# Performance work log

Measured on AMD Instinct MI355X. Metric: run time of the kernel, lower is better.

The kernel has to match this reference:

```python
import jax, jax.numpy as jnp
import numpy as np

B, M, N = 32, 512, 512
XD = YD = 512   # x_size, y_size
S = 512         # shared_size
H = 512         # hidden_size
MAXD = 11       # max relative distance


def _lin(k, i, o):
    lim = float(np.sqrt(6.0 / (i + o)))  # xavier_uniform, gain=1
    return jax.random.uniform(k, (i, o), jnp.float32, -lim, lim)


def setup_inputs() -> dict:
    key = jax.random.key(0)
    ks = jax.random.split(key, 16)
    inp = {
        'prem': jax.random.normal(ks[0], (B, M, YD), jnp.float32),
        'hypo': jax.random.normal(ks[1], (B, N, XD), jnp.float32),
        'prem_mask': jnp.ones((B, M), dtype=bool),
        'hypo_mask': jnp.ones((B, N), dtype=bool),
        # projections
        'Wpx': _lin(ks[2], XD, S), 'bpx': jnp.zeros((S,), jnp.float32),
        'Wpy': _lin(ks[3], YD, S), 'bpy': jnp.zeros((S,), jnp.float32),
        # relative-distance bias embedding (2*max_dist+1, squeezed to scalar)
        'dist_embed': jax.random.normal(ks[4], (2 * MAXD + 1,), jnp.float32),
        # self-attention DeepDot MLP: S -> H -> H
        'Ws1': _lin(ks[5], S, H), 'bs1': jnp.zeros((H,), jnp.float32),
        'Ws2': _lin(ks[6], H, H), 'bs2': jnp.zeros((H,), jnp.float32),
        # cross-attention DeepDot MLP: 2S -> H -> H
        'Wa1': _lin(ks[7], 2 * S, H), 'ba1': jnp.zeros((H,), jnp.float32),
        'Wa2': _lin(ks[8], H, H), 'ba2': jnp.zeros((H,), jnp.float32),
        # compare layer: 4S -> H -> H
        'Wc1': _lin(ks[9], 4 * S, H), 'bc1': jnp.zeros((H,), jnp.float32),
        'Wc2': _lin(ks[10], H, H), 'bc2': jnp.zeros((H,), jnp.float32),
        # aggregate layer: 2H -> H -> H
        'Wg1': _lin(ks[11], 2 * H, H), 'bg1': jnp.zeros((H,), jnp.float32),
        'Wg2': _lin(ks[12], H, H), 'bg2': jnp.zeros((H,), jnp.float32),
    }
    return inp


def _mlp2(x, W1, b1, W2, b2):
    # Linear -> ReLU -> Linear -> ReLU (dropout=0.0)
    h = jax.nn.relu(x @ W1 + b1)
    return jax.nn.relu(h @ W2 + b2)


def _rel_bias(size, dist_embed):
    v = jnp.arange(size)
    d = jnp.clip(v[None, :] - v[:, None], -MAXD, MAXD) + MAXD  # [size,size]
    return dist_embed[d]


def _masked_softmax(t, mask):
    # mask True = valid; broadcast over query dim
    return jax.nn.softmax(jnp.where(mask, t, -jnp.inf), axis=-1)


def reference(prem, hypo, prem_mask, hypo_mask,
              Wpx, bpx, Wpy, bpy, dist_embed,
              Ws1, bs1, Ws2, bs2,
              Wa1, ba1, Wa2, ba2,
              Wc1, bc1, Wc2, bc2,
              Wg1, bg1, Wg2, bg2):
    hypo_p = hypo @ Wpx + bpx   # [B,N,S]
    prem_p = prem @ Wpy + bpy   # [B,M,S]

    # self attention (DeepDot: shared MLP on q and k, then qk^T)
    fp = _mlp2(prem_p, Ws1, bs1, Ws2, bs2)
    fh = _mlp2(hypo_p, Ws1, bs1, Ws2, bs2)
    p_scores = jnp.einsum('bmh,bnh->bmn', fp, fp) + _rel_bias(prem_p.shape[1], dist_embed)[None]
    h_scores = jnp.einsum('bmh,bnh->bmn', fh, fh) + _rel_bias(hypo_p.shape[1], dist_embed)[None]

    p_att = _masked_softmax(p_scores, prem_mask[:, None, :])
    h_att = _masked_softmax(h_scores, hypo_mask[:, None, :])
    prem_ctx = jnp.einsum('bmn,bnd->bmd', p_att, prem_p)
    hypo_ctx = jnp.einsum('bmn,bnd->bmd', h_att, hypo_p)

    prem2 = jnp.concatenate([prem_p, prem_ctx], axis=-1)  # [B,M,2S]
    hypo2 = jnp.concatenate([hypo_p, hypo_ctx], axis=-1)  # [B,N,2S]

    # cross attention
    gp = _mlp2(prem2, Wa1, ba1, Wa2, ba2)
    gh = _mlp2(hypo2, Wa1, ba1, Wa2, ba2)
    sim = jnp.einsum('bmh,bnh->bmn', gp, gh)  # [B,M,N]
    p2h = _masked_softmax(sim, hypo_mask[:, None, :])
    h2p = _masked_softmax(jnp.swapaxes(sim, 1, 2), prem_mask[:, None, :])
    attended_hypo = jnp.einsum('bmn,bnd->bmd', p2h, hypo2)  # [B,M,2S]
    attended_prem = jnp.einsum('bnm,bmd->bnd', h2p, prem2)  # [B,N,2S]

    prem_cmp = _mlp2(jnp.concatenate([prem2, attended_hypo], -1), Wc1, bc1, Wc2, bc2)
    hypo_cmp = _mlp2(jnp.concatenate([hypo2, attended_prem], -1), Wc1, bc1, Wc2, bc2)

    prem_cmp = (prem_cmp * prem_mask[..., None].astype(prem_cmp.dtype)).sum(axis=1)  # [B,H]
    hypo_cmp = (hypo_cmp * hypo_mask[..., None].astype(hypo_cmp.dtype)).sum(axis=1)  # [B,H]

    return _mlp2(jnp.concatenate([prem_cmp, hypo_cmp], -1), Wg1, bg1, Wg2, bg2)
```

## Files before the change

kernel.cpp:

```cpp
#include <hip/hip_runtime.h>
#include <hip/hip_bf16.h>


typedef __bf16 bf16x8 __attribute__((ext_vector_type(8)));
typedef float floatx16 __attribute__((ext_vector_type(16)));
typedef float floatx4 __attribute__((ext_vector_type(4)));

__device__ __forceinline__ unsigned short f32_to_bf16(float f) {
    unsigned int u = __float_as_uint(f);
    unsigned int r = (u + 0x7FFFu + ((u >> 16) & 1u)) >> 16;
    return (unsigned short)r;
}
__device__ __forceinline__ float bf16_to_f32(unsigned short h) {
    return __uint_as_float(((unsigned int)h) << 16);
}

__device__ __forceinline__ void gload16(const void* g, void* l) {
    __builtin_amdgcn_global_load_lds(
        (const __attribute__((address_space(1))) unsigned int*)g,
        (__attribute__((address_space(3))) unsigned int*)l, 16, 0, 0);
}

#define FENCE_BAR() do { asm volatile("" ::: "memory"); \
    __builtin_amdgcn_s_barrier(); \
    asm volatile("" ::: "memory"); } while (0)

struct TW {
    const float* src[8];
    unsigned short* dst[8];
    int K[8];
};
__global__ __launch_bounds__(256) void transpose_all_kernel(TW tw) {
    const int z = blockIdx.z;
    const int K = tw.K[z];
    const int k0 = blockIdx.y * 32;
    if (k0 >= K) return;
    const float* W = tw.src[z];
    unsigned short* Wt = tw.dst[z];
    __shared__ unsigned short tile[32][33];
    int n0 = blockIdx.x * 32;
    int tx = threadIdx.x & 31, ty = threadIdx.x >> 5;
    #pragma unroll
    for (int i = 0; i < 4; ++i) {
        int ky = ty + i * 8;
        tile[ky][tx] = f32_to_bf16(W[(long long)(k0 + ky) * 512 + n0 + tx]);
    }
    __syncthreads();
    #pragma unroll
    for (int i = 0; i < 4; ++i) {
        int ny = ty + i * 8;
        Wt[(long long)(n0 + ny) * K + k0 + tx] = tile[tx][ny];
    }
}

template <bool BT, bool AF32>
__global__ __launch_bounds__(256, 4) void gemm_kernel(
    const void* __restrict__ Av, const void* __restrict__ A2v, int lda, long long strideA,
    const unsigned short* __restrict__ Bw, int ldb, long long strideB, int bxor,
    const unsigned short* __restrict__ B2, const float* __restrict__ bias2, int Msplit,
    float* __restrict__ C32, unsigned short* __restrict__ Cb, int ldc, long long strideC,
    const float* __restrict__ bias, int relu, int M, int N, int K,
    float* __restrict__ csum, int swz) {
    constexpr int BBYTES = BT ? 8192 : (32 * 264);
    constexpr int BUF = 8192 + BBYTES;
    __shared__ alignas(16) char smem[2 * BUF];

    const int t = threadIdx.x;
    const int lane = t & 63;
    const int wave = t >> 6;
    const int wm = (wave >> 1) * 64;
    const int wn = (wave & 1) * 64;
    const int ln = lane & 31;
    const int h = lane >> 5;

    int bx = blockIdx.x, by = blockIdx.y, bz = blockIdx.z;
    if (swz == 1) {
        int Nt = gridDim.x, Mt = gridDim.y;
        int L = by * Nt + bx;
        int x = L & 7, s = L >> 3;
        by = x * (Mt >> 3) + s / Nt;
        bx = s % Nt;
    } else if (swz == 2) {
        int Nt = gridDim.x, Mt = gridDim.y;
        int L = (bz * Mt + by) * Nt + bx;
        int x = L & 7, s = L >> 3;
        int mg = x * ((Mt * (int)gridDim.z) >> 3) + s / Nt;
        bx = s % Nt;
        by = mg % Mt;
        bz = mg / Mt;
    }
    const int m0 = by * 128;
    const int n0 = bx * 128;
    const int bzB = (bz + bxor) & ((int)gridDim.z - 1);

    const unsigned short* B = Bw;
    const float* biasp = bias;
    long long mA = m0;
    if (Msplit && m0 >= Msplit) {
        if (B2) B = B2;
        if (bias2) biasp = bias2;
        if (A2v) { Av = A2v; mA = m0 - Msplit; }
    }

    const float* aptrF = nullptr;
    const unsigned short* aptrH = nullptr;
    if constexpr (AF32)
        aptrF = (const float*)Av + (long long)bz * strideA +
                (mA + (t >> 1)) * (long long)lda + (t & 1) * 16;
    else
        aptrH = (const unsigned short*)Av + (long long)bz * strideA +
                (mA + (t >> 1)) * (long long)lda + (t & 1) * 16;
    const unsigned short* bptr;
    if (BT)
        bptr = B + (long long)bzB * strideB +
               (long long)(n0 + (t >> 1)) * ldb + (t & 1) * 16;
    else
        bptr = B + (long long)bzB * strideB +
               (long long)(t >> 4) * ldb + n0 + (t & 15) * 8;
    const long long bstep = BT ? 8 : 16 * (long long)ldb;

    const int aoff = ((t & 1) * 256 + (t >> 1)) * 16;
    const int boff = BT ? (8192 + ((t & 1) * 256 + (t >> 1)) * 16)
                        : (8192 + (t >> 4) * 264 + (t & 15) * 16);
    const int boff2 = BT ? 2048 : 16 * 264;

    floatx16 acc[2][2];
    #pragma unroll
    for (int im = 0; im < 2; ++im)
        #pragma unroll
        for (int in = 0; in < 2; ++in)
            acc[im][in] = (floatx16)(0.f);

    uint4 va0, va1, vb0, vb1;
    float4 fa0, fa1, fa2, fa3;

    auto loadA = [&]() {
        if constexpr (AF32) {
            fa0 = *(const float4*)(aptrF);
            fa1 = *(const float4*)(aptrF + 4);
            fa2 = *(const float4*)(aptrF + 8);
            fa3 = *(const float4*)(aptrF + 12);
            aptrF += 32;
        } else {
            va0 = *(const uint4*)(aptrH);
            va1 = *(const uint4*)(aptrH + 8);
            aptrH += 32;
        }
    };
    auto loadB = [&]() {
        vb0 = *(const uint4*)(bptr);
        vb1 = *(const uint4*)(bptr + bstep);
        bptr += BT ? 32 : 32 * (long long)ldb;
    };
    auto commit = [&](char* buf) {
        if constexpr (AF32) {
            union { uint4 q; unsigned short u[8]; } c0, c1;
            c0.u[0] = f32_to_bf16(fa0.x); c0.u[1] = f32_to_bf16(fa0.y);
            c0.u[2] = f32_to_bf16(fa0.z); c0.u[3] = f32_to_bf16(fa0.w);
            c0.u[4] = f32_to_bf16(fa1.x); c0.u[5] = f32_to_bf16(fa1.y);
            c0.u[6] = f32_to_bf16(fa1.z); c0.u[7] = f32_to_bf16(fa1.w);
            c1.u[0] = f32_to_bf16(fa2.x); c1.u[1] = f32_to_bf16(fa2.y);
            c1.u[2] = f32_to_bf16(fa2.z); c1.u[3] = f32_to_bf16(fa2.w);
            c1.u[4] = f32_to_bf16(fa3.x); c1.u[5] = f32_to_bf16(fa3.y);
            c1.u[6] = f32_to_bf16(fa3.z); c1.u[7] = f32_to_bf16(fa3.w);
            *(uint4*)(buf + aoff) = c0.q;
            *(uint4*)(buf + aoff + 2048) = c1.q;
        } else {
            *(uint4*)(buf + aoff) = va0;
            *(uint4*)(buf + aoff + 2048) = va1;
        }
        *(uint4*)(buf + boff) = vb0;
        *(uint4*)(buf + boff + boff2) = vb1;
    };

    loadA(); loadB();
    commit(smem);
    loadA(); loadB();
    __syncthreads();

    int p = 0;
    for (int k0 = 0; k0 < K; k0 += 32) {
        const char* base = smem + p * BUF;
        #pragma unroll
        for (int s = 0; s < 2; ++s) {
            bf16x8 a[2], b[2];
            #pragma unroll
            for (int im = 0; im < 2; ++im)
                a[im] = *(const bf16x8*)(base + ((s * 2 + h) * 128 + wm + im * 32 + ln) * 16);
            if (BT) {
                #pragma unroll
                for (int in = 0; in < 2; ++in)
                    b[in] = *(const bf16x8*)(base + 8192 +
                                             ((s * 2 + h) * 128 + wn + in * 32 + ln) * 16);
            } else {
                #pragma unroll
                for (int in = 0; in < 2; ++in) {
                    union { bf16x8 v; unsigned short u[8]; } u;
                    #pragma unroll
                    for (int j = 0; j < 8; ++j)
                        u.u[j] = *(const unsigned short*)(base + 8192 +
                                 (s * 16 + h * 8 + j) * 264 + (wn + in * 32 + ln) * 2);
                    b[in] = u.v;
                }
            }
            #pragma unroll
            for (int im = 0; im < 2; ++im)
                #pragma unroll
                for (int in = 0; in < 2; ++in)
                    acc[im][in] = __builtin_amdgcn_mfma_f32_32x32x16_bf16(
                        a[im], b[in], acc[im][in], 0, 0, 0);
        }

        if (k0 + 32 < K) {
            commit(smem + (p ^ 1) * BUF);
            if (k0 + 64 < K) { loadA(); loadB(); }
            __syncthreads();
            p ^= 1;
        }
    }

    if (csum) {
        const int bidx = m0 >> 9;
        const long long cbase = (long long)(bidx & 31) * 1024 + (bidx >> 5) * 512;
        #pragma unroll
        for (int in = 0; in < 2; ++in) {
            int n = n0 + wn + in * 32 + ln;
            float bn = biasp ? biasp[n] : 0.f;
            float s = 0.f;
            #pragma unroll
            for (int im = 0; im < 2; ++im)
                #pragma unroll
                for (int r = 0; r < 16; ++r) {
                    float v = acc[im][in][r] + bn;
                    if (relu) v = fmaxf(v, 0.f);
                    s += v;
                }
            s += __shfl_xor(s, 32);
            if (lane < 32) atomicAdd(&csum[cbase + n], s);
        }
        return;
    }

    float* C32b = C32 ? C32 + (long long)bz * strideC : nullptr;
    unsigned short* Cbb = Cb ? Cb + (long long)bz * strideC : nullptr;
    #pragma unroll
    for (int im = 0; im < 2; ++im) {
        #pragma unroll
        for (int in = 0; in < 2; ++in) {
            int n = n0 + wn + in * 32 + ln;
            float bn = biasp ? biasp[n] : 0.f;
            #pragma unroll
            for (int r = 0; r < 16; ++r) {
                int m = m0 + wm + im * 32 + (r & 3) + 8 * (r >> 2) + 4 * h;
                float v = acc[im][in][r] + bn;
                if (relu) v = fmaxf(v, 0.f);
                long long off = (long long)m * ldc + n;
                if (C32b) C32b[off] = v;
                if (Cbb) Cbb[off] = f32_to_bf16(v);
            }
        }
    }
}

__global__ __launch_bounds__(512, 2) void gemm256_kernel(
    const unsigned short* __restrict__ Aw, int lda, long long strideA,
    const unsigned short* __restrict__ Bw, int ldb, long long strideB, int bxor,
    float* __restrict__ C32, unsigned short* __restrict__ Cb, int ldc, long long strideC,
    const float* __restrict__ bias, int relu, int K) {
    extern __shared__ __align__(16) char smem[];

    const int tid = threadIdx.x;
    const int lane = tid & 63;
    const int wave = tid >> 6;
    const int wr = wave >> 2;
    const int wc = wave & 3;

    int bx = blockIdx.x, by = blockIdx.y, bz = blockIdx.z;
    {
        const int gx = gridDim.x, gy = gridDim.y;
        const int nwg = gx * gy * (int)gridDim.z;
        if ((nwg & 7) == 0) {
            int L = (bz * gy + by) * gx + bx;
            int flat = (L & 7) * (nwg >> 3) + (L >> 3);
            bx = flat % gx;
            int R = flat / gx;
            by = R % gy;
            bz = R / gy;
        }
    }
    const int m0 = by * 256;
    const int n0 = bx * 256;
    const int bzB = (bz + bxor) & ((int)gridDim.z - 1);

    const int rowT = tid >> 3;
    const int chS = (tid & 7) ^ (rowT & 7);
    const long long ldaB = (long long)lda * 2;
    const long long ldbB = (long long)ldb * 2;
    const char* aG = (const char*)Aw +
        ((long long)bz * strideA + (long long)(m0 + rowT) * lda) * 2 + chS * 16;
    const char* bG = (const char*)Bw +
        ((long long)bzB * strideB + (long long)(n0 + rowT) * ldb) * 2 + chS * 16;
    const int dOff = tid * 16;

    auto stA = [&](int tt, int h) {
        const char* g = aG + (long long)(h * 128) * ldaB + (long long)tt * 128;
        char* l = smem + (tt & 1) * 65536 + h * 16384 + dOff;
        gload16(g, l);
        gload16(g + 64 * ldaB, l + 8192);
    };
    auto stB = [&](int tt, int h) {
        const char* g = bG + (long long)(h * 128) * ldbB + (long long)tt * 128;
        char* l = smem + (tt & 1) * 65536 + 32768 + h * 16384 + dOff;
        gload16(g, l);
        gload16(g + 64 * ldbB, l + 8192);
    };

    const int l15 = lane & 15;
    const int lk = lane >> 4;
    const int swzb = (lane & 7) << 4;
    const int c0 = (lk * 16) ^ swzb;
    const int c1 = (64 + lk * 16) ^ swzb;
    const int arow = (wr * 128 + l15) * 128;
    const int brow = 32768 + (wc * 64 + l15) * 128;

    floatx4 acc[8][4];
    #pragma unroll
    for (int mf = 0; mf < 8; ++mf)
        #pragma unroll
        for (int nf = 0; nf < 4; ++nf)
            acc[mf][nf] = (floatx4)(0.f);

    const int NT = K >> 6;

    stA(0, 0); stA(0, 1); stB(0, 0); stB(0, 1);
    if (NT > 1) {
        stB(1, 0); stB(1, 1);
        asm volatile("s_waitcnt vmcnt(4)" ::: "memory");
    } else {
        asm volatile("s_waitcnt vmcnt(0)" ::: "memory");
    }
    FENCE_BAR();

    bf16x8 a[4][2], b[4][2];
    for (int t = 0; t < NT; ++t) {
        const char* buf = smem + (t & 1) * 65536;
        const char* aB = buf + arow;
        const char* bB = buf + brow;

        #pragma unroll
        for (int mf = 0; mf < 4; ++mf) {
            a[mf][0] = *(const bf16x8*)(aB + mf * 2048 + c0);
            a[mf][1] = *(const bf16x8*)(aB + mf * 2048 + c1);
        }
        #pragma unroll
        for (int nf = 0; nf < 2; ++nf) {
            b[nf][0] = *(const bf16x8*)(bB + nf * 2048 + c0);
            b[nf][1] = *(const bf16x8*)(bB + nf * 2048 + c1);
        }
        if (t + 1 < NT) stA(t + 1, 0);
        FENCE_BAR();
        __builtin_amdgcn_s_setprio(1);
        #pragma unroll
        for (int mf = 0; mf < 4; ++mf)
            #pragma unroll
            for (int nf = 0; nf < 2; ++nf) {
                acc[mf][nf] = __builtin_amdgcn_mfma_f32_16x16x32_bf16(
                    a[mf][0], b[nf][0], acc[mf][nf], 0, 0, 0);
                acc[mf][nf] = __builtin_amdgcn_mfma_f32_16x16x32_bf16(
                    a[mf][1], b[nf][1], acc[mf][nf], 0, 0, 0);
            }
        __builtin_amdgcn_s_setprio(0);
        FENCE_BAR();

        #pragma unroll
        for (int nf = 2; nf < 4; ++nf) {
            b[nf][0] = *(const bf16x8*)(bB + nf * 2048 + c0);
            b[nf][1] = *(const bf16x8*)(bB + nf * 2048 + c1);
        }
        if (t + 1 < NT) stA(t + 1, 1);
        FENCE_BAR();
        __builtin_amdgcn_s_setprio(1);
        #pragma unroll
        for (int mf = 0; mf < 4; ++mf)
            #pragma unroll
            for (int nf = 2; nf < 4; ++nf) {
                acc[mf][nf] = __builtin_amdgcn_mfma_f32_16x16x32_bf16(
                    a[mf][0], b[nf][0], acc[mf][nf], 0, 0, 0);
                acc[mf][nf] = __builtin_amdgcn_mfma_f32_16x16x32_bf16(
                    a[mf][1], b[nf][1], acc[mf][nf], 0, 0, 0);
            }
        __builtin_amdgcn_s_setprio(0);
        FENCE_BAR();

        #pragma unroll
        for (int mf = 0; mf < 4; ++mf) {
            a[mf][0] = *(const bf16x8*)(aB + (4 + mf) * 2048 + c0);
            a[mf][1] = *(const bf16x8*)(aB + (4 + mf) * 2048 + c1);
        }
        if (t + 2 < NT) stB(t + 2, 0);
        FENCE_BAR();
        __builtin_amdgcn_s_setprio(1);
        #pragma unroll
        for (int mf = 0; mf < 4; ++mf)
            #pragma unroll
            for (int nf = 2; nf < 4; ++nf) {
                acc[4 + mf][nf] = __builtin_amdgcn_mfma_f32_16x16x32_bf16(
                    a[mf][0], b[nf][0], acc[4 + mf][nf], 0, 0, 0);
                acc[4 + mf][nf] = __builtin_amdgcn_mfma_f32_16x16x32_bf16(
                    a[mf][1], b[nf][1], acc[4 + mf][nf], 0, 0, 0);
            }
        __builtin_amdgcn_s_setprio(0);
        FENCE_BAR();

        if (t + 2 < NT) {
            stB(t + 2, 1);
            asm volatile("s_waitcnt vmcnt(4)" ::: "memory");
        } else {
            asm volatile("s_waitcnt vmcnt(0)" ::: "memory");
        }
        FENCE_BAR();
        __builtin_amdgcn_s_setprio(1);
        #pragma unroll
        for (int mf = 0; mf < 4; ++mf)
            #pragma unroll
            for (int nf = 0; nf < 2; ++nf) {
                acc[4 + mf][nf] = __builtin_amdgcn_mfma_f32_16x16x32_bf16(
                    a[mf][0], b[nf][0], acc[4 + mf][nf], 0, 0, 0);
                acc[4 + mf][nf] = __builtin_amdgcn_mfma_f32_16x16x32_bf16(
                    a[mf][1], b[nf][1], acc[4 + mf][nf], 0, 0, 0);
            }
        __builtin_amdgcn_s_setprio(0);
        FENCE_BAR();
    }

    const int rg = (lane >> 4) * 4;
    float* C32b = C32 ? C32 + (long long)bz * strideC : nullptr;
    unsigned short* Cbb = Cb ? Cb + (long long)bz * strideC : nullptr;
    #pragma unroll
    for (int nf = 0; nf < 4; ++nf) {
        const int n = n0 + wc * 64 + nf * 16 + l15;
        const float bn = bias ? bias[n] : 0.f;
        #pragma unroll
        for (int mf = 0; mf < 8; ++mf) {
            #pragma unroll
            for (int r = 0; r < 4; ++r) {
                int m = m0 + wr * 128 + mf * 16 + rg + r;
                float v = acc[mf][nf][r] + bn;
                if (relu) v = fmaxf(v, 0.f);
                long long off = (long long)m * ldc + n;
                if (C32b) C32b[off] = v;
                if (Cbb) Cbb[off] = f32_to_bf16(v);
            }
        }
    }
}

__global__ __launch_bounds__(256, 2) void attn_kernel(
    const unsigned short* __restrict__ F,
    int bxor,
    unsigned short* __restrict__ att,
    const float* __restrict__ de, int rel) {
    constexpr int BUF = 36864;
    __shared__ alignas(16) char smem[2 * BUF];
    __shared__ alignas(16) float red[2][64][4];
    __shared__ float deL[23];

    const int t = threadIdx.x;
    const int lane = t & 63;
    const int wave = t >> 6;
    const int ln = lane & 31;
    const int h = lane >> 5;

    const int orig = blockIdx.y * (int)gridDim.x + blockIdx.x;
    const int xcd = orig & 7;
    const int s8 = orig >> 3;
    const int by = s8 & 7;
    const int bz = xcd + ((s8 >> 3) << 3);
    const int m0 = by * 64;
    const int bzB = (bz + bxor) & 63;

    if (t < 23) deL[t] = de[t];

    const unsigned short* aptr = F + (long long)bz * (512 * 512) +
                                 (m0 + (t >> 2)) * 512 + (t & 3) * 8;
    const unsigned short* bptr = F + (long long)bzB * (512 * 512) +
                                 (t >> 1) * 512 + (t & 1) * 16;
    const int aoff = ((t & 3) * 64 + (t >> 2)) * 16;
    const int c2 = (t & 1) * 2;
    const int brow = (t >> 1) * 16;

    floatx16 acc[2][4];
    #pragma unroll
    for (int mf = 0; mf < 2; ++mf)
        #pragma unroll
        for (int nf = 0; nf < 4; ++nf)
            acc[mf][nf] = (floatx16)(0.f);

    uint4 qa, q0a, q0b, q1a, q1b, q2a, q2b, q3a, q3b;
    auto load = [&]() {
        qa  = *(const uint4*)(aptr);
        q0a = *(const uint4*)(bptr);
        q0b = *(const uint4*)(bptr + 8);
        q1a = *(const uint4*)(bptr + 65536);
        q1b = *(const uint4*)(bptr + 65536 + 8);
        q2a = *(const uint4*)(bptr + 131072);
        q2b = *(const uint4*)(bptr + 131072 + 8);
        q3a = *(const uint4*)(bptr + 196608);
        q3b = *(const uint4*)(bptr + 196608 + 8);
        aptr += 32; bptr += 32;
    };
    auto commit = [&](char* buf) {
        *(uint4*)(buf + aoff) = qa;
        char* bb = buf + 4096;
        *(uint4*)(bb + (c2 + 0) * 8192 + brow) = q0a;
        *(uint4*)(bb + (c2 + 1) * 8192 + brow) = q0b;
        *(uint4*)(bb + (c2 + 0) * 8192 + brow + 128 * 16) = q1a;
        *(uint4*)(bb + (c2 + 1) * 8192 + brow + 128 * 16) = q1b;
        *(uint4*)(bb + (c2 + 0) * 8192 + brow + 256 * 16) = q2a;
        *(uint4*)(bb + (c2 + 1) * 8192 + brow + 256 * 16) = q2b;
        *(uint4*)(bb + (c2 + 0) * 8192 + brow + 384 * 16) = q3a;
        *(uint4*)(bb + (c2 + 1) * 8192 + brow + 384 * 16) = q3b;
    };

    load(); commit(smem); load();
    __syncthreads();

    int p = 0;
    for (int k0 = 0; k0 < 512; k0 += 32) {
        const char* buf = smem + p * BUF;
        #pragma unroll
        for (int s = 0; s < 2; ++s) {
            bf16x8 a[2], b[4];
            #pragma unroll
            for (int mf = 0; mf < 2; ++mf)
                a[mf] = *(const bf16x8*)(buf + ((s * 2 + h) * 64 + mf * 32 + ln) * 16);
            #pragma unroll
            for (int nf = 0; nf < 4; ++nf)
                b[nf] = *(const bf16x8*)(buf + 4096 + (s * 2 + h) * 8192 +
                                         (wave * 128 + nf * 32 + ln) * 16);
            #pragma unroll
            for (int mf = 0; mf < 2; ++mf)
                #pragma unroll
                for (int nf = 0; nf < 4; ++nf)
                    acc[mf][nf] = __builtin_amdgcn_mfma_f32_32x32x16_bf16(
                        a[mf], b[nf], acc[mf][nf], 0, 0, 0);
        }
        if (k0 + 32 < 512) {
            commit(smem + (p ^ 1) * BUF);
            if (k0 + 64 < 512) load();
            __syncthreads();
            p ^= 1;
        }
    }

    if (rel) {
        #pragma unroll
        for (int mf = 0; mf < 2; ++mf)
            #pragma unroll
            for (int nf = 0; nf < 4; ++nf)
                #pragma unroll
                for (int r = 0; r < 16; ++r) {
                    int row = m0 + mf * 32 + (r & 3) + 8 * (r >> 2) + 4 * h;
                    int col = wave * 128 + nf * 32 + ln;
                    int d = min(11, max(-11, col - row));
                    acc[mf][nf][r] += deL[d + 11];
                }
    }

    #pragma unroll
    for (int mf = 0; mf < 2; ++mf)
        #pragma unroll
        for (int r = 0; r < 16; ++r) {
            float mx = fmaxf(fmaxf(acc[mf][0][r], acc[mf][1][r]),
                             fmaxf(acc[mf][2][r], acc[mf][3][r]));
            #pragma unroll
            for (int o = 16; o > 0; o >>= 1) mx = fmaxf(mx, __shfl_xor(mx, o));
            if (ln == 0)
                red[0][mf * 32 + (r & 3) + 8 * (r >> 2) + 4 * h][wave] = mx;
        }
    __syncthreads();

    #pragma unroll
    for (int mf = 0; mf < 2; ++mf)
        #pragma unroll
        for (int r = 0; r < 16; ++r) {
            const int rl = mf * 32 + (r & 3) + 8 * (r >> 2) + 4 * h;
            float4 q = *(const float4*)red[0][rl];
            float mx = fmaxf(fmaxf(q.x, q.y), fmaxf(q.z, q.w));
            float s = 0.f;
            #pragma unroll
            for (int nf = 0; nf < 4; ++nf) {
                acc[mf][nf][r] = __expf(acc[mf][nf][r] - mx);
                s += acc[mf][nf][r];
            }
            #pragma unroll
            for (int o = 16; o > 0; o >>= 1) s += __shfl_xor(s, o);
            if (ln == 0) red[1][rl][wave] = s;
        }
    __syncthreads();

    unsigned short* ab = att + ((long long)bz * 512 + m0) * 1024;
    #pragma unroll
    for (int mf = 0; mf < 2; ++mf)
        #pragma unroll
        for (int r = 0; r < 16; ++r) {
            const int rl = mf * 32 + (r & 3) + 8 * (r >> 2) + 4 * h;
            float4 q = *(const float4*)red[1][rl];
            float inv = 1.f / (q.x + q.y + q.z + q.w);
            #pragma unroll
            for (int nf = 0; nf < 4; ++nf) {
                int col = wave * 128 + nf * 32 + ln;
                ab[(long long)rl * 1024 + col] = f32_to_bf16(acc[mf][nf][r] * inv);
            }
        }
}

__global__ __launch_bounds__(512) void mlp_agg_kernel(const float* __restrict__ X,
                                                      const float* __restrict__ W,
                                                      const float* __restrict__ bias,
                                                      float* __restrict__ out,
                                                      int K, int N, int relu) {
    const int b = blockIdx.y;
    const int nl = threadIdx.x & 63;
    const int n = blockIdx.x * 64 + nl;
    const int ks = threadIdx.x >> 6;
    const int kchunk = K >> 3;
    const float* Xb = X + (long long)b * K;
    const int k0 = ks * kchunk;
    float s = 0.f;
    #pragma unroll 8
    for (int k = k0; k < k0 + kchunk; ++k)
        s += Xb[k] * W[(long long)k * N + n];
    __shared__ float red[8][64];
    red[ks][nl] = s;
    __syncthreads();
    if (threadIdx.x < 64) {
        float t = 0.f;
        #pragma unroll
        for (int i = 0; i < 8; ++i) t += red[i][threadIdx.x];
        t += bias[n];
        if (relu) t = fmaxf(t, 0.f);
        out[(long long)b * N + n] = t;
    }
}

static void gemm(hipStream_t st, bool bt, bool af32,
                 const void* A, const void* A2, int lda, long long sA,
                 const void* B, int ldb, long long sB, int bxor,
                 const void* B2, const float* bias2, int Msplit,
                 float* C32, void* Cb, int ldc, long long sC,
                 const float* bias, int relu, int M, int N, int K, int batch,
                 float* csum = nullptr) {
    dim3 g(N / 128, M / 128, batch), blk(256);
    int swz = 0;
    if (batch == 1 && (M / 128) % 8 == 0) swz = 1;
    else if (batch > 1 && ((M / 128) * batch) % 8 == 0) swz = 2;
    if (bt) {
        if (af32)
            gemm_kernel<true, true><<<g, blk, 0, st>>>(
                A, A2, lda, sA, (const unsigned short*)B, ldb, sB, bxor,
                (const unsigned short*)B2, bias2, Msplit,
                C32, (unsigned short*)Cb, ldc, sC, bias, relu, M, N, K, csum, swz);
        else
            gemm_kernel<true, false><<<g, blk, 0, st>>>(
                A, A2, lda, sA, (const unsigned short*)B, ldb, sB, bxor,
                (const unsigned short*)B2, bias2, Msplit,
                C32, (unsigned short*)Cb, ldc, sC, bias, relu, M, N, K, csum, swz);
    } else {
        gemm_kernel<false, false><<<g, blk, 0, st>>>(
            A, A2, lda, sA, (const unsigned short*)B, ldb, sB, bxor,
            (const unsigned short*)B2, bias2, Msplit,
            C32, (unsigned short*)Cb, ldc, sC, bias, relu, M, N, K, csum, swz);
    }
}

static void gemm256(hipStream_t st,
                    const void* A, int lda, long long sA,
                    const void* B, int ldb, long long sB, int bxor,
                    float* C32, void* Cb, int ldc, long long sC,
                    const float* bias, int relu, int M, int N, int K, int batch) {
    static bool inited = false;
    if (!inited) {
        hipFuncSetAttribute(reinterpret_cast<const void*>(gemm256_kernel),
                            hipFuncAttributeMaxDynamicSharedMemorySize, 131072);
        inited = true;
    }
    dim3 g(N / 256, M / 256, batch);
    gemm256_kernel<<<g, 512, 131072, st>>>(
        (const unsigned short*)A, lda, sA,
        (const unsigned short*)B, ldb, sB, bxor,
        C32, (unsigned short*)Cb, ldc, sC, bias, relu, K);
}

extern "C" void kernel_launch(void* const* d_in, const int* in_sizes, int n_in,
                              void* d_out, int out_size, void* d_ws, size_t ws_size,
                              hipStream_t stream) {
    const int B = 32, SEQ = 512;
    const int MT = B * SEQ;
    const int M2 = 2 * MT;

    const float* prem = (const float*)d_in[0];
    const float* hypo = (const float*)d_in[1];
    const float* Wpx = (const float*)d_in[4];  const float* bpx = (const float*)d_in[5];
    const float* Wpy = (const float*)d_in[6];  const float* bpy = (const float*)d_in[7];
    const float* de  = (const float*)d_in[8];
    const float* Ws1 = (const float*)d_in[9];  const float* bs1 = (const float*)d_in[10];
    const float* Ws2 = (const float*)d_in[11]; const float* bs2 = (const float*)d_in[12];
    const float* Wa1 = (const float*)d_in[13]; const float* ba1 = (const float*)d_in[14];
    const float* Wa2 = (const float*)d_in[15]; const float* ba2 = (const float*)d_in[16];
    const float* Wc1 = (const float*)d_in[17]; const float* bc1 = (const float*)d_in[18];
    const float* Wc2 = (const float*)d_in[19]; const float* bc2 = (const float*)d_in[20];
    const float* Wg1 = (const float*)d_in[21]; const float* bg1 = (const float*)d_in[22];
    const float* Wg2 = (const float*)d_in[23]; const float* bg2 = (const float*)d_in[24];

    char* p = (char*)d_ws;
    auto alloc = [&](size_t bytes) { char* r = p; p += (bytes + 255) & ~(size_t)255; return r; };
    unsigned short* prem_bf = (unsigned short*)alloc((size_t)MT * 512 * 2);
    unsigned short* hypo_bf = (unsigned short*)alloc((size_t)MT * 512 * 2);
    unsigned short* premcat = (unsigned short*)alloc((size_t)MT * 2048 * 2);
    unsigned short* hypocat = (unsigned short*)alloc((size_t)MT * 2048 * 2);
    float* scores = (float*)alloc((size_t)64 * SEQ * SEQ * 4);
    unsigned short* h1 = (unsigned short*)scores;
    unsigned short* att = (unsigned short*)scores;
    unsigned short* Wpx_t = (unsigned short*)alloc(512 * 512 * 2);
    unsigned short* Wpy_t = (unsigned short*)alloc(512 * 512 * 2);
    unsigned short* Ws1_t = (unsigned short*)alloc(512 * 512 * 2);
    unsigned short* Ws2_t = (unsigned short*)alloc(512 * 512 * 2);
    unsigned short* Wa1_t = (unsigned short*)alloc(512 * 1024 * 2);
    unsigned short* Wa2_t = (unsigned short*)alloc(512 * 512 * 2);
    unsigned short* Wc1_t = (unsigned short*)alloc(512 * 2048 * 2);
    unsigned short* Wc2_t = (unsigned short*)alloc(512 * 512 * 2);
    float* agg  = (float*)alloc(32 * 1024 * 4);
    float* aggh = (float*)alloc(32 * 512 * 4);
    (void)hypo_bf; (void)hypocat; (void)scores;

    const long long sBM = (long long)SEQ * SEQ;
    const long long sAtt = (long long)SEQ * 1024;
    const long long sCat = (long long)SEQ * 2048;

    {
        TW tw;
        tw.src[0] = Wpy; tw.dst[0] = Wpy_t; tw.K[0] = 512;
        tw.src[1] = Wpx; tw.dst[1] = Wpx_t; tw.K[1] = 512;
        tw.src[2] = Ws1; tw.dst[2] = Ws1_t; tw.K[2] = 512;
        tw.src[3] = Ws2; tw.dst[3] = Ws2_t; tw.K[3] = 512;
        tw.src[4] = Wa1; tw.dst[4] = Wa1_t; tw.K[4] = 1024;
        tw.src[5] = Wa2; tw.dst[5] = Wa2_t; tw.K[5] = 512;
        tw.src[6] = Wc1; tw.dst[6] = Wc1_t; tw.K[6] = 2048;
        tw.src[7] = Wc2; tw.dst[7] = Wc2_t; tw.K[7] = 512;
        transpose_all_kernel<<<dim3(16, 64, 8), 256, 0, stream>>>(tw);
        hipMemsetAsync(agg, 0, 32 * 1024 * sizeof(float), stream);
    }

    gemm(stream, true, true, prem, hypo, 512, 0, Wpy_t, 512, 0, 0,
         Wpx_t, bpx, MT, nullptr, premcat, 2048, 0, bpy, 0, M2, 512, 512, 1);

    gemm256(stream, premcat, 2048, 0, Ws1_t, 512, 0, 0,
            nullptr, h1, 512, 0, bs1, 1, M2, 512, 512, 1);
    gemm256(stream, h1, 512, 0, Ws2_t, 512, 0, 0,
            nullptr, prem_bf, 512, 0, bs2, 1, M2, 512, 512, 1);

    attn_kernel<<<dim3(8, 64), 256, 0, stream>>>(prem_bf, 0, att, de, 1);
    gemm(stream, false, false, att, nullptr, 1024, sAtt, premcat, 2048, sCat, 0,
         nullptr, nullptr, 0, nullptr, premcat + 512, 2048, sCat, nullptr, 0, 512, 512, 512, 64);

    gemm256(stream, premcat, 2048, 0, Wa1_t, 1024, 0, 0,
            nullptr, h1, 512, 0, ba1, 1, M2, 512, 1024, 1);
    gemm256(stream, h1, 512, 0, Wa2_t, 512, 0, 0,
            nullptr, prem_bf, 512, 0, ba2, 1, M2, 512, 512, 1);

    attn_kernel<<<dim3(8, 64), 256, 0, stream>>>(prem_bf, 32, att, de, 0);
    gemm(stream, false, false, att, nullptr, 1024, sAtt, premcat, 2048, sCat, 32,
         nullptr, nullptr, 0, nullptr, premcat + 1024, 2048, sCat, nullptr, 0, 512, 1024, 512, 64);

    gemm256(stream, premcat, 2048, 0, Wc1_t, 2048, 0, 0,
            nullptr, h1, 512, 0, bc1, 1, M2, 512, 2048, 1);
    gemm(stream, true, false, h1, nullptr, 512, 0, Wc2_t, 512, 0, 0,
         nullptr, nullptr, 0, nullptr, nullptr, 512, 0, bc2, 1, M2, 512, 512, 1, agg);

    mlp_agg_kernel<<<dim3(8, 32), 512, 0, stream>>>(agg, Wg1, bg1, aggh, 1024, 512, 1);
    mlp_agg_kernel<<<dim3(8, 32), 512, 0, stream>>>(aggh, Wg2, bg2, (float*)d_out, 512, 512, 1);
}
```

Before: 622.2 us.

## Fuse softmax probabilities with the PV matmul in one attention kernel

Result: slower. 673.9 us (+8.3%).

```diff
diff --git a/kernel.cpp b/kernel.cpp
--- a/kernel.cpp
+++ b/kernel.cpp
@@ -455,14 +455,25 @@
     }
 }
 
-__global__ __launch_bounds__(256, 2) void attn_kernel(
+template <bool CROSS>
+__global__ __launch_bounds__(512, 1) void attnpv_kernel(
     const unsigned short* __restrict__ F,
+    const unsigned short* __restrict__ Vsrc,
     int bxor,
-    unsigned short* __restrict__ att,
+    unsigned short* __restrict__ ctxout,
     const float* __restrict__ de, int rel) {
-    constexpr int BUF = 36864;
-    __shared__ alignas(16) char smem[2 * BUF];
-    __shared__ alignas(16) float red[2][64][4];
+    constexpr int D   = CROSS ? 1024 : 512;
+    constexpr int KS  = CROSS ? 16 : 32;
+    constexpr int NS  = 512 / KS;
+    constexpr int VP  = CROSS ? 2080 : 1056;
+    constexpr int DS  = CROSS ? 4 : 2;
+    constexpr int WD  = CROSS ? 128 : 64;
+    constexpr int PBASE = 66560;
+    constexpr int VBYTES = KS * VP;
+    constexpr int SBUF = 36864;
+
+    extern __shared__ __align__(16) char smem[];
+    __shared__ float red[2][64][8];
     __shared__ float deL[23];
 
     const int t = threadIdx.x;
@@ -483,43 +494,33 @@
 
     const unsigned short* aptr = F + (long long)bz * (512 * 512) +
                                  (m0 + (t >> 2)) * 512 + (t & 3) * 8;
-    const unsigned short* bptr = F + (long long)bzB * (512 * 512) +
-                                 (t >> 1) * 512 + (t & 1) * 16;
+    const unsigned short* bptr = F + (long long)bzB * (512 * 512) + t * 512;
     const int aoff = ((t & 3) * 64 + (t >> 2)) * 16;
-    const int c2 = (t & 1) * 2;
-    const int brow = (t >> 1) * 16;
-
-    floatx16 acc[2][4];
+    const int boffB = t * 16;
+
+    floatx16 acc[2][2];
     #pragma unroll
     for (int mf = 0; mf < 2; ++mf)
         #pragma unroll
-        for (int nf = 0; nf < 4; ++nf)
+        for (int nf = 0; nf < 2; ++nf)
             acc[mf][nf] = (floatx16)(0.f);
 
-    uint4 qa, q0a, q0b, q1a, q1b, q2a, q2b, q3a, q3b;
+    uint4 qa, qb0, qb1, qb2, qb3;
     auto load = [&]() {
-        qa  = *(const uint4*)(aptr);
-        q0a = *(const uint4*)(bptr);
-        q0b = *(const uint4*)(bptr + 8);
-        q1a = *(const uint4*)(bptr + 65536);
-        q1b = *(const uint4*)(bptr + 65536 + 8);
-        q2a = *(const uint4*)(bptr + 131072);
-        q2b = *(const uint4*)(bptr + 131072 + 8);
-        q3a = *(const uint4*)(bptr + 196608);
-        q3b = *(const uint4*)(bptr + 196608 + 8);
+        if (t < 256) qa = *(const uint4*)(aptr);
+        qb0 = *(const uint4*)(bptr);
+        qb1 = *(const uint4*)(bptr + 8);
+        qb2 = *(const uint4*)(bptr + 16);
+        qb3 = *(const uint4*)(bptr + 24);
         aptr += 32; bptr += 32;
     };
     auto commit = [&](char* buf) {
-        *(uint4*)(buf + aoff) = qa;
+        if (t < 256) *(uint4*)(buf + aoff) = qa;
         char* bb = buf + 4096;
-        *(uint4*)(bb + (c2 + 0) * 8192 + brow) = q0a;
-        *(uint4*)(bb + (c2 + 1) * 8192 + brow) = q0b;
-        *(uint4*)(bb + (c2 + 0) * 8192 + brow + 128 * 16) = q1a;
-        *(uint4*)(bb + (c2 + 1) * 8192 + brow + 128 * 16) = q1b;
-        *(uint4*)(bb + (c2 + 0) * 8192 + brow + 256 * 16) = q2a;
-        *(uint4*)(bb + (c2 + 1) * 8192 + brow + 256 * 16) = q2b;
-        *(uint4*)(bb + (c2 + 0) * 8192 + brow + 384 * 16) = q3a;
-        *(uint4*)(bb + (c2 + 1) * 8192 + brow + 384 * 16) = q3b;
+        *(uint4*)(bb + 0 * 8192 + boffB) = qb0;
+        *(uint4*)(bb + 1 * 8192 + boffB) = qb1;
+        *(uint4*)(bb + 2 * 8192 + boffB) = qb2;
+        *(uint4*)(bb + 3 * 8192 + boffB) = qb3;
     };
 
     load(); commit(smem); load();
@@ -527,26 +528,26 @@
 
     int p = 0;
     for (int k0 = 0; k0 < 512; k0 += 32) {
-        const char* buf = smem + p * BUF;
+        const char* buf = smem + p * SBUF;
         #pragma unroll
         for (int s = 0; s < 2; ++s) {
-            bf16x8 a[2], b[4];
+            bf16x8 a[2], b[2];
             #pragma unroll
             for (int mf = 0; mf < 2; ++mf)
                 a[mf] = *(const bf16x8*)(buf + ((s * 2 + h) * 64 + mf * 32 + ln) * 16);
             #pragma unroll
-            for (int nf = 0; nf < 4; ++nf)
+            for (int nf = 0; nf < 2; ++nf)
                 b[nf] = *(const bf16x8*)(buf + 4096 + (s * 2 + h) * 8192 +
-                                         (wave * 128 + nf * 32 + ln) * 16);
+                                         (wave * 64 + nf * 32 + ln) * 16);
             #pragma unroll
             for (int mf = 0; mf < 2; ++mf)
                 #pragma unroll
-                for (int nf = 0; nf < 4; ++nf)
+                for (int nf = 0; nf < 2; ++nf)
                     acc[mf][nf] = __builtin_amdgcn_mfma_f32_32x32x16_bf16(
                         a[mf], b[nf], acc[mf][nf], 0, 0, 0);
         }
         if (k0 + 32 < 512) {
-            commit(smem + (p ^ 1) * BUF);
+            commit(smem + (p ^ 1) * SBUF);
             if (k0 + 64 < 512) load();
             __syncthreads();
             p ^= 1;
@@ -557,11 +558,11 @@
         #pragma unroll
         for (int mf = 0; mf < 2; ++mf)
             #pragma unroll
-            for (int nf = 0; nf < 4; ++nf)
+            for (int nf = 0; nf < 2; ++nf)
                 #pragma unroll
                 for (int r = 0; r < 16; ++r) {
                     int row = m0 + mf * 32 + (r & 3) + 8 * (r >> 2) + 4 * h;
-                    int col = wave * 128 + nf * 32 + ln;
+                    int col = wave * 64 + nf * 32 + ln;
                     int d = min(11, max(-11, col - row));
                     acc[mf][nf][r] += deL[d + 11];
                 }
@@ -571,8 +572,7 @@
     for (int mf = 0; mf < 2; ++mf)
         #pragma unroll
         for (int r = 0; r < 16; ++r) {
-            float mx = fmaxf(fmaxf(acc[mf][0][r], acc[mf][1][r]),
-                             fmaxf(acc[mf][2][r], acc[mf][3][r]));
+            float mx = fmaxf(acc[mf][0][r], acc[mf][1][r]);
             #pragma unroll
             for (int o = 16; o > 0; o >>= 1) mx = fmaxf(mx, __shfl_xor(mx, o));
             if (ln == 0)
@@ -585,11 +585,13 @@
         #pragma unroll
         for (int r = 0; r < 16; ++r) {
             const int rl = mf * 32 + (r & 3) + 8 * (r >> 2) + 4 * h;
-            float4 q = *(const float4*)red[0][rl];
-            float mx = fmaxf(fmaxf(q.x, q.y), fmaxf(q.z, q.w));
+            float4 qm0 = *(const float4*)&red[0][rl][0];
+            float4 qm1 = *(const float4*)&red[0][rl][4];
+            float mx = fmaxf(fmaxf(fmaxf(qm0.x, qm0.y), fmaxf(qm0.z, qm0.w)),
+                             fmaxf(fmaxf(qm1.x, qm1.y), fmaxf(qm1.z, qm1.w)));
             float s = 0.f;
             #pragma unroll
-            for (int nf = 0; nf < 4; ++nf) {
+            for (int nf = 0; nf < 2; ++nf) {
                 acc[mf][nf][r] = __expf(acc[mf][nf][r] - mx);
                 s += acc[mf][nf][r];
             }
@@ -599,18 +601,100 @@
         }
     __syncthreads();
 
-    unsigned short* ab = att + ((long long)bz * 512 + m0) * 1024;
+    const unsigned short* vG = Vsrc + (long long)bzB * (512 * 2048);
+    const int vrow = CROSS ? (t >> 5) : (t >> 4);
+    const int vch = (CROSS ? (t & 31) : (t & 15)) * 4;
+    const unsigned short* vptr = vG + (long long)vrow * 2048 + vch * 8;
+    uint4 v0, v1, v2, v3;
+    auto vload = [&](int s) {
+        const unsigned short* g = vptr + (long long)s * KS * 2048;
+        v0 = *(const uint4*)(g);
+        v1 = *(const uint4*)(g + 8);
+        v2 = *(const uint4*)(g + 16);
+        v3 = *(const uint4*)(g + 24);
+    };
+    auto vcommit = [&](int vb) {
+        char* b = smem + PBASE + vb * VBYTES + vrow * VP + vch * 16;
+        *(uint4*)(b) = v0;
+        *(uint4*)(b + 16) = v1;
+        *(uint4*)(b + 32) = v2;
+        *(uint4*)(b + 48) = v3;
+    };
+
+    vload(0);
+
     #pragma unroll
     for (int mf = 0; mf < 2; ++mf)
         #pragma unroll
         for (int r = 0; r < 16; ++r) {
             const int rl = mf * 32 + (r & 3) + 8 * (r >> 2) + 4 * h;
-            float4 q = *(const float4*)red[1][rl];
-            float inv = 1.f / (q.x + q.y + q.z + q.w);
-            #pragma unroll
-            for (int nf = 0; nf < 4; ++nf) {
-                int col = wave * 128 + nf * 32 + ln;
-                ab[(long long)rl * 1024 + col] = f32_to_bf16(acc[mf][nf][r] * inv);
+            float4 qs0 = *(const float4*)&red[1][rl][0];
+            float4 qs1 = *(const float4*)&red[1][rl][4];
+            float inv = 1.f / (qs0.x + qs0.y + qs0.z + qs0.w +
+                               qs1.x + qs1.y + qs1.z + qs1.w);
+            #pragma unroll
+            for (int nf = 0; nf < 2; ++nf) {
+                int key = wave * 64 + nf * 32 + ln;
+                *(unsigned short*)(smem + rl * 1040 + key * 2) =
+                    f32_to_bf16(acc[mf][nf][r] * inv);
+            }
+        }
+    __syncthreads();
+
+    vcommit(0);
+    if (NS > 1) vload(1);
+    __syncthreads();
+
+    floatx16 pacc[2][DS];
+    #pragma unroll
+    for (int mf = 0; mf < 2; ++mf)
+        #pragma unroll
+        for (int df = 0; df < DS; ++df)
+            pacc[mf][df] = (floatx16)(0.f);
+
+    int vp = 0;
+    for (int s = 0; s < NS; ++s) {
+        const char* Vb = smem + PBASE + vp * VBYTES;
+        const int kk0 = s * KS;
+        #pragma unroll
+        for (int ks = 0; ks < KS / 16; ++ks) {
+            bf16x8 pa[2];
+            #pragma unroll
+            for (int mf = 0; mf < 2; ++mf)
+                pa[mf] = *(const bf16x8*)(smem + (mf * 32 + ln) * 1040 +
+                                          (kk0 + ks * 16 + h * 8) * 2);
+            #pragma unroll
+            for (int df = 0; df < DS; ++df) {
+                union { bf16x8 v; unsigned short u[8]; } vb;
+                #pragma unroll
+                for (int j = 0; j < 8; ++j)
+                    vb.u[j] = *(const unsigned short*)(Vb +
+                              (ks * 16 + h * 8 + j) * VP +
+                              (wave * WD + df * 32 + ln) * 2);
+                #pragma unroll
+                for (int mf = 0; mf < 2; ++mf)
+                    pacc[mf][df] = __builtin_amdgcn_mfma_f32_32x32x16_bf16(
+                        pa[mf], vb.v, pacc[mf][df], 0, 0, 0);
+            }
+        }
+        if (s + 1 < NS) {
+            vcommit(vp ^ 1);
+            if (s + 2 < NS) vload(s + 2);
+        }
+        __syncthreads();
+        vp ^= 1;
+    }
+
+    unsigned short* cb = ctxout + ((long long)bz * 512 + m0) * 2048;
+    #pragma unroll
+    for (int mf = 0; mf < 2; ++mf)
+        #pragma unroll
+        for (int r = 0; r < 16; ++r) {
+            const int q = mf * 32 + (r & 3) + 8 * (r >> 2) + 4 * h;
+            #pragma unroll
+            for (int df = 0; df < DS; ++df) {
+                int col = wave * WD + df * 32 + ln;
+                cb[(long long)q * 2048 + col] = f32_to_bf16(pacc[mf][df][r]);
             }
         }
 }
@@ -721,7 +805,6 @@
     unsigned short* hypocat = (unsigned short*)alloc((size_t)MT * 2048 * 2);
     float* scores = (float*)alloc((size_t)64 * SEQ * SEQ * 4);
     unsigned short* h1 = (unsigned short*)scores;
-    unsigned short* att = (unsigned short*)scores;
     unsigned short* Wpx_t = (unsigned short*)alloc(512 * 512 * 2);
     unsigned short* Wpy_t = (unsigned short*)alloc(512 * 512 * 2);
     unsigned short* Ws1_t = (unsigned short*)alloc(512 * 512 * 2);
@@ -734,11 +817,17 @@
     float* aggh = (float*)alloc(32 * 512 * 4);
     (void)hypo_bf; (void)hypocat; (void)scores;
 
-    const long long sBM = (long long)SEQ * SEQ;
-    const long long sAtt = (long long)SEQ * 1024;
     const long long sCat = (long long)SEQ * 2048;
 
     {
+        static bool inited = false;
+        if (!inited) {
+            hipFuncSetAttribute(reinterpret_cast<const void*>(attnpv_kernel<false>),
+                                hipFuncAttributeMaxDynamicSharedMemorySize, 134144);
+            hipFuncSetAttribute(reinterpret_cast<const void*>(attnpv_kernel<true>),
+                                hipFuncAttributeMaxDynamicSharedMemorySize, 134144);
+            inited = true;
+        }
         TW tw;
         tw.src[0] = Wpy; tw.dst[0] = Wpy_t; tw.K[0] = 512;
         tw.src[1] = Wpx; tw.dst[1] = Wpx_t; tw.K[1] = 512;
@@ -760,18 +849,16 @@
     gemm256(stream, h1, 512, 0, Ws2_t, 512, 0, 0,
             nullptr, prem_bf, 512, 0, bs2, 1, M2, 512, 512, 1);
 
-    attn_kernel<<<dim3(8, 64), 256, 0, stream>>>(prem_bf, 0, att, de, 1);
-    gemm(stream, false, false, att, nullptr, 1024, sAtt, premcat, 2048, sCat, 0,
-         nullptr, nullptr, 0, nullptr, premcat + 512, 2048, sCat, nullptr, 0, 512, 512, 512, 64);
+    attnpv_kernel<false><<<dim3(8, 64), 512, 134144, stream>>>(
+        prem_bf, premcat, 0, premcat + 512, de, 1);
 
     gemm256(stream, premcat, 2048, 0, Wa1_t, 1024, 0, 0,
             nullptr, h1, 512, 0, ba1, 1, M2, 512, 1024, 1);
     gemm256(stream, h1, 512, 0, Wa2_t, 512, 0, 0,
             nullptr, prem_bf, 512, 0, ba2, 1, M2, 512, 512, 1);
 
-    attn_kernel<<<dim3(8, 64), 256, 0, stream>>>(prem_bf, 32, att, de, 0);
-    gemm(stream, false, false, att, nullptr, 1024, sAtt, premcat, 2048, sCat, 32,
-         nullptr, nullptr, 0, nullptr, premcat + 1024, 2048, sCat, nullptr, 0, 512, 1024, 512, 64);
+    attnpv_kernel<true><<<dim3(8, 64), 512, 134144, stream>>>(
+        prem_bf, premcat, 32, premcat + 1024, de, 0);
 
     gemm256(stream, premcat, 2048, 0, Wc1_t, 2048, 0, 0,
             nullptr, h1, 512, 0, bc1, 1, M2, 512, 2048, 1);
```
